# Kernel optimization log

Measured on AMD Instinct MI355X. Metric: run time of the kernel, lower is better.

The kernel has to match this reference:

```python
import jax, jax.numpy as jnp
import numpy as np

CW = 64            # channel_width; N = CW**2 = 4096 tokens = d_batch
BIAS = 1.0         # same_channel_bias
D_KQ = 2048
D_V = 2048
STEP = 0           # self.step at first call
T_IDX = 0          # self.t at first call
PE_N = 10000.0


def pe_row(t, d, n=PE_N):
    """Row t of the sinusoidal positional encoding P[t, :] of width d (d even)."""
    i = jnp.arange(d // 2, dtype=jnp.float32)
    denom = jnp.power(jnp.float32(n), 2.0 * i / d)
    ang = jnp.float32(t) / denom
    row = jnp.zeros((d,), dtype=jnp.float32)
    row = row.at[0::2].set(jnp.sin(ang)).at[1::2].set(jnp.cos(ang))
    return row


def setup_inputs() -> dict:
    key = jax.random.key(0)
    ks = jax.random.split(key, 6)
    N = CW * CW          # 4096
    d_in = 2048
    num_steps = 8
    return {
        "x": jax.random.normal(ks[0], (N, d_in), dtype=jnp.float32),
        "W_query": jax.random.uniform(ks[1], (d_in, D_KQ), dtype=jnp.float32),
        "W_key": jax.random.uniform(ks[2], (d_in, D_KQ), dtype=jnp.float32),
        "W_value": jax.random.uniform(ks[3], (d_in, D_V), dtype=jnp.float32),
        "b_channel": jax.random.uniform(ks[4], (N, D_V), dtype=jnp.float32),
        "b_t": jax.random.uniform(ks[5], (num_steps, N, D_V), dtype=jnp.float32),
    }


def reference(x, W_query, W_key, W_value, b_channel, b_t):
    N = x.shape[0]
    q = x @ W_query                      # [N, d_kq]
    k = x @ W_key                        # [N, d_kq]
    v = x @ W_value                      # [N, d_v]
    scores = q @ k.T                     # [N, N]
    # kron(eye(cw), ones(cw,cw)*bias): +bias where tokens share a channel block
    ch = jnp.arange(N) // CW
    scores = scores + jnp.where(ch[:, None] == ch[None, :], jnp.float32(BIAS), jnp.float32(0.0))
    # NOTE: bias added BEFORE the 1/sqrt(d_kq) scaling, as in the original
    attn = jax.nn.softmax(scores / jnp.float32(D_KQ) ** 0.5, axis=-1)
    ctx = attn @ v                       # [N, d_v]
    ctx = ctx + b_channel + b_t[STEP] + pe_row(T_IDX, D_V)
    return ctx
```

## Files before the change

### kernel.cpp

```cpp
#include <hip/hip_runtime.h>
#include <cstdint>
#include <cstddef>


using h8    = __attribute__((ext_vector_type(8))) _Float16;
using h4    = __attribute__((ext_vector_type(4))) _Float16;
using f32x4 = __attribute__((ext_vector_type(4))) float;

__device__ __forceinline__ void gll16(const void* g, void* l) {
  __builtin_amdgcn_global_load_lds(
      (const __attribute__((address_space(1))) uint32_t*)g,
      (__attribute__((address_space(3))) uint32_t*)l, 16, 0, 0);
}

__global__ __launch_bounds__(256) void split_x_kernel(
    const float* __restrict__ X, _Float16* __restrict__ hi,
    _Float16* __restrict__ lo, int n4)
{
  int i = blockIdx.x * 256 + threadIdx.x;
  if (i >= n4) return;
  float4 v = ((const float4*)X)[i];
  float a[4] = {v.x, v.y, v.z, v.w};
  h4 hh, ll;
#pragma unroll
  for (int e = 0; e < 4; ++e) {
    _Float16 h = (_Float16)a[e];
    hh[e] = h;
    ll[e] = (_Float16)(a[e] - (float)h);
  }
  ((h4*)hi)[i] = hh;
  ((h4*)lo)[i] = ll;
}

__global__ __launch_bounds__(256) void transpose_split_w(
    const float* __restrict__ W, _Float16* __restrict__ Thi,
    _Float16* __restrict__ Tlo, int D, int writeLo)
{
  __shared__ float t[32][33];
  int n0 = blockIdx.x * 32;
  int k0 = blockIdx.y * 32;
  int tx = threadIdx.x & 31;
  int ty = threadIdx.x >> 5;
  for (int j = ty; j < 32; j += 8)
    t[j][tx] = W[(size_t)(k0 + j) * D + n0 + tx];
  __syncthreads();
  for (int j = ty; j < 32; j += 8) {
    float v = t[tx][j];
    size_t o = (size_t)(n0 + j) * D + k0 + tx;
    _Float16 h = (_Float16)v;
    Thi[o] = h;
    if (writeLo) Tlo[o] = (_Float16)(v - (float)h);
  }
}

constexpr int EPI_QK = 0;
constexpr int EPI_VT = 1;
constexpr int EPI_S  = 2;
constexpr int EPI_CTX = 3;

template<int EPI, bool SPLIT>
__global__ __launch_bounds__(256, 2) void gemm_bt(
    const _Float16* __restrict__ A, const _Float16* __restrict__ Al,
    const _Float16* __restrict__ B, const _Float16* __restrict__ Bl,
    int K, int lda, int ldb, int ldc, int ldt,
    float* __restrict__ of32, _Float16* __restrict__ oh1,
    _Float16* __restrict__ oh2,
    const float* __restrict__ c1, const float* __restrict__ c2)
{
  __shared__ __align__(16) _Float16 sA [128 * 32];
  __shared__ __align__(16) _Float16 sB [128 * 32];
  __shared__ __align__(16) _Float16 sAl[SPLIT ? 128 * 32 : 8];
  __shared__ __align__(16) _Float16 sBl[SPLIT ? 128 * 32 : 8];

  const int tid  = threadIdx.x;
  const int lane = tid & 63;
  const int wave = tid >> 6;
  const int wm = wave >> 1, wn = wave & 1;
  const int m0 = blockIdx.y * 128, n0 = blockIdx.x * 128;

  const int ca = lane + 64 * wave;
  const int ra = ca >> 2, ka = (ca & 3) * 8;
  const int cc = ca + 256;
  const int rb = cc >> 2, kb = (cc & 3) * 8;
  const size_t lo0 = (size_t)wave * 1024;
  const size_t lo1 = lo0 + 4096;

  const _Float16* gA0 = A + (size_t)(m0 + ra) * lda + ka;
  const _Float16* gA1 = A + (size_t)(m0 + rb) * lda + kb;
  const _Float16* gB0 = B + (size_t)(n0 + ra) * ldb + ka;
  const _Float16* gB1 = B + (size_t)(n0 + rb) * ldb + kb;
  const _Float16* gAl0 = Al ? Al + (size_t)(m0 + ra) * lda + ka : nullptr;
  const _Float16* gAl1 = Al ? Al + (size_t)(m0 + rb) * lda + kb : nullptr;
  const _Float16* gBl0 = Bl ? Bl + (size_t)(n0 + ra) * ldb + ka : nullptr;
  const _Float16* gBl1 = Bl ? Bl + (size_t)(n0 + rb) * ldb + kb : nullptr;

  f32x4 acc[4][4];
#pragma unroll
  for (int i = 0; i < 4; ++i)
#pragma unroll
    for (int j = 0; j < 4; ++j) acc[i][j] = (f32x4){0.f, 0.f, 0.f, 0.f};

  const int fr = lane & 15;
  const int fk = (lane >> 4) * 8;

  for (int k0 = 0; k0 < K; k0 += 32) {
    gll16(gA0 + k0, (char*)sA + lo0);
    gll16(gA1 + k0, (char*)sA + lo1);
    gll16(gB0 + k0, (char*)sB + lo0);
    gll16(gB1 + k0, (char*)sB + lo1);
    if constexpr (SPLIT) {
      gll16(gAl0 + k0, (char*)sAl + lo0);
      gll16(gAl1 + k0, (char*)sAl + lo1);
      gll16(gBl0 + k0, (char*)sBl + lo0);
      gll16(gBl1 + k0, (char*)sBl + lo1);
    }
    __syncthreads();

    h8 af[4], bf[4], afl[4], bfl[4];
#pragma unroll
    for (int mi = 0; mi < 4; ++mi)
      af[mi] = *(const h8*)&sA[(wm * 64 + mi * 16 + fr) * 32 + fk];
#pragma unroll
    for (int ni = 0; ni < 4; ++ni)
      bf[ni] = *(const h8*)&sB[(wn * 64 + ni * 16 + fr) * 32 + fk];
    if constexpr (SPLIT) {
#pragma unroll
      for (int mi = 0; mi < 4; ++mi)
        afl[mi] = *(const h8*)&sAl[(wm * 64 + mi * 16 + fr) * 32 + fk];
#pragma unroll
      for (int ni = 0; ni < 4; ++ni)
        bfl[ni] = *(const h8*)&sBl[(wn * 64 + ni * 16 + fr) * 32 + fk];
    }

#pragma unroll
    for (int mi = 0; mi < 4; ++mi)
#pragma unroll
      for (int ni = 0; ni < 4; ++ni) {
        acc[mi][ni] = __builtin_amdgcn_mfma_f32_16x16x32_f16(
            af[mi], bf[ni], acc[mi][ni], 0, 0, 0);
        if constexpr (SPLIT) {
          acc[mi][ni] = __builtin_amdgcn_mfma_f32_16x16x32_f16(
              af[mi], bfl[ni], acc[mi][ni], 0, 0, 0);
          acc[mi][ni] = __builtin_amdgcn_mfma_f32_16x16x32_f16(
              afl[mi], bf[ni], acc[mi][ni], 0, 0, 0);
        }
      }
    __syncthreads();
  }

  const int drow = (lane >> 4) * 4;
  const int dcol = lane & 15;
#pragma unroll
  for (int mi = 0; mi < 4; ++mi) {
#pragma unroll
    for (int ni = 0; ni < 4; ++ni) {
      const int row = m0 + wm * 64 + mi * 16 + drow;
      const int col = n0 + wn * 64 + ni * 16 + dcol;
      f32x4 v = acc[mi][ni];
      if constexpr (EPI == EPI_S) {
#pragma unroll
        for (int r = 0; r < 4; ++r)
          of32[(size_t)(row + r) * ldc + col] = v[r];
      } else if constexpr (EPI == EPI_QK) {
#pragma unroll
        for (int r = 0; r < 4; ++r) {
          float x = v[r];
          _Float16 hh = (_Float16)x;
          size_t o = (size_t)(row + r) * ldc + col;
          oh1[o] = hh;
          oh2[o] = (_Float16)(x - (float)hh);
        }
      } else if constexpr (EPI == EPI_VT) {
        h4 hh;
#pragma unroll
        for (int r = 0; r < 4; ++r) hh[r] = (_Float16)v[r];
        *(h4*)&oh1[(size_t)col * ldt + row] = hh;
      } else {
#pragma unroll
        for (int r = 0; r < 4; ++r) {
          size_t o = (size_t)(row + r) * ldc + col;
          of32[o] = v[r] + c1[o] + c2[o] + ((col & 1) ? 1.0f : 0.0f);
        }
      }
    }
  }
}

template<int EPI, int NPASS>
__global__ __launch_bounds__(512, 2) void gemm256(
    const _Float16* __restrict__ A0, const _Float16* __restrict__ B0,
    const _Float16* __restrict__ A1, const _Float16* __restrict__ B1,
    const _Float16* __restrict__ A2, const _Float16* __restrict__ B2,
    int lda, int ldb, int ldc,
    float* __restrict__ of32, _Float16* __restrict__ oh1,
    _Float16* __restrict__ oh2)
{
  __shared__ __align__(16) char lds[147456];
  constexpr int T = NPASS * 32;

  const int tid  = threadIdx.x;
  const int lane = tid & 63;
  const int w    = tid >> 6;
  const int wm = w >> 2, wn = w & 3;
  const int fr = lane & 15, sl = lane >> 4;
  const int m0 = blockIdx.y * 256, n0 = blockIdx.x * 256;

  const int sswz  = ((sl ^ ((fr >> 1) & 3)) << 4);
  const int aBase = (wm * 128 + fr) * 64 + sswz;
  const int bBase = 65536 + (wn * 64 + fr) * 64 + sswz;
  const int rowoff = w * 16 + (lane >> 2);
  const int sL8 = ((lane & 3) ^ ((lane >> 3) & 3)) * 8;

  auto gstage = [&](int t, int isB, int kk) {
    const _Float16* g; int ld, r0, gk; char* dst;
    if (t >= T) {
      g = A0; ld = lda; r0 = m0; gk = 0; dst = lds + 131072;
    } else {
      const int p = t >> 5, kt = t & 31;
      g  = isB ? (p == 0 ? B0 : (p == 1 ? B1 : B2))
               : (p == 0 ? A0 : (p == 1 ? A1 : A2));
      ld = isB ? ldb : lda;
      r0 = isB ? n0 : m0;
      gk = kt * 64 + kk * 32;
      dst = lds + (isB ? 65536 : 0) + (t & 1) * 32768 + kk * 16384;
    }
#pragma unroll
    for (int i = 0; i < 2; ++i)
      gll16(g + (size_t)(r0 + i * 128 + rowoff) * ld + gk + sL8,
            dst + i * 8192 + w * 1024);
  };

  f32x4 acc[8][4];
#pragma unroll
  for (int i = 0; i < 8; ++i)
#pragma unroll
    for (int j = 0; j < 4; ++j) acc[i][j] = (f32x4){0.f, 0.f, 0.f, 0.f};

  gstage(0, 0, 0); gstage(0, 1, 0);
  gstage(0, 0, 1); gstage(0, 1, 1);
  gstage(1, 0, 0); gstage(1, 1, 0);
  asm volatile("s_waitcnt vmcnt(8)" ::: "memory");
  __builtin_amdgcn_sched_barrier(0);
  __builtin_amdgcn_s_barrier();

  h8 af[4], bf[4];
#pragma unroll 2
  for (int t = 0; t < T; ++t) {
    const char* aB = lds + (t & 1) * 32768;

#pragma unroll
    for (int i = 0; i < 4; ++i) af[i] = *(const h8*)(aB + aBase + i * 1024);
#pragma unroll
    for (int i = 0; i < 4; ++i) bf[i] = *(const h8*)(aB + bBase + i * 1024);
    gstage(t + 1, 0, 1);
    __builtin_amdgcn_s_barrier();
    asm volatile("s_waitcnt lgkmcnt(0)" ::: "memory");
    __builtin_amdgcn_sched_barrier(0);
    __builtin_amdgcn_s_setprio(1);
#pragma unroll
    for (int mi = 0; mi < 4; ++mi)
#pragma unroll
      for (int ni = 0; ni < 4; ++ni)
        acc[mi][ni] = __builtin_amdgcn_mfma_f32_16x16x32_f16(
            af[mi], bf[ni], acc[mi][ni], 0, 0, 0);
    __builtin_amdgcn_s_setprio(0);
    __builtin_amdgcn_s_barrier();

#pragma unroll
    for (int i = 0; i < 4; ++i)
      af[i] = *(const h8*)(aB + aBase + (4 + i) * 1024);
    gstage(t + 1, 1, 1);
    __builtin_amdgcn_s_barrier();
    asm volatile("s_waitcnt lgkmcnt(0)" ::: "memory");
    __builtin_amdgcn_sched_barrier(0);
    __builtin_amdgcn_s_setprio(1);
#pragma unroll
    for (int mi = 0; mi < 4; ++mi)
#pragma unroll
      for (int ni = 0; ni < 4; ++ni)
        acc[4 + mi][ni] = __builtin_amdgcn_mfma_f32_16x16x32_f16(
            af[mi], bf[ni], acc[4 + mi][ni], 0, 0, 0);
    __builtin_amdgcn_s_setprio(0);
    asm volatile("s_waitcnt vmcnt(8)" ::: "memory");
    __builtin_amdgcn_sched_barrier(0);
    __builtin_amdgcn_s_barrier();

#pragma unroll
    for (int i = 0; i < 4; ++i)
      af[i] = *(const h8*)(aB + 16384 + aBase + i * 1024);
#pragma unroll
    for (int i = 0; i < 4; ++i)
      bf[i] = *(const h8*)(aB + 16384 + bBase + i * 1024);
    gstage(t + 2, 0, 0);
    __builtin_amdgcn_s_barrier();
    asm volatile("s_waitcnt lgkmcnt(0)" ::: "memory");
    __builtin_amdgcn_sched_barrier(0);
    __builtin_amdgcn_s_setprio(1);
#pragma unroll
    for (int mi = 0; mi < 4; ++mi)
#pragma unroll
      for (int ni = 0; ni < 4; ++ni)
        acc[mi][ni] = __builtin_amdgcn_mfma_f32_16x16x32_f16(
            af[mi], bf[ni], acc[mi][ni], 0, 0, 0);
    __builtin_amdgcn_s_setprio(0);
    __builtin_amdgcn_s_barrier();

#pragma unroll
    for (int i = 0; i < 4; ++i)
      af[i] = *(const h8*)(aB + 16384 + aBase + (4 + i) * 1024);
    gstage(t + 2, 1, 0);
    __builtin_amdgcn_s_barrier();
    asm volatile("s_waitcnt lgkmcnt(0)" ::: "memory");
    __builtin_amdgcn_sched_barrier(0);
    __builtin_amdgcn_s_setprio(1);
#pragma unroll
    for (int mi = 0; mi < 4; ++mi)
#pragma unroll
      for (int ni = 0; ni < 4; ++ni)
        acc[4 + mi][ni] = __builtin_amdgcn_mfma_f32_16x16x32_f16(
            af[mi], bf[ni], acc[4 + mi][ni], 0, 0, 0);
    __builtin_amdgcn_s_setprio(0);
    asm volatile("s_waitcnt vmcnt(8)" ::: "memory");
    __builtin_amdgcn_sched_barrier(0);
    __builtin_amdgcn_s_barrier();
  }
  asm volatile("s_waitcnt vmcnt(0)" ::: "memory");

  const int drow = sl * 4;
#pragma unroll
  for (int mi = 0; mi < 8; ++mi) {
#pragma unroll
    for (int ni = 0; ni < 4; ++ni) {
      const int row = m0 + wm * 128 + mi * 16 + drow;
      const int col = n0 + wn * 64 + ni * 16 + fr;
      f32x4 v = acc[mi][ni];
      if constexpr (EPI == EPI_S) {
#pragma unroll
        for (int r = 0; r < 4; ++r)
          of32[(size_t)(row + r) * ldc + col] = v[r];
      } else {
#pragma unroll
        for (int r = 0; r < 4; ++r) {
          float x = v[r];
          _Float16 hh = (_Float16)x;
          size_t o = (size_t)(row + r) * ldc + col;
          oh1[o] = hh;
          oh2[o] = (_Float16)(x - (float)hh);
        }
      }
    }
  }
}

__global__ __launch_bounds__(256) void softmax_bias_kernel(
    float* __restrict__ S, int N)
{
  const float scale = 0.022097086912079608f;
  const int row = blockIdx.x;
  float* rp = S + (size_t)row * N;
  const int cblk = row & ~63;
  const int tid = threadIdx.x;

  float vals[16];
  float mx = -3.0e38f;
#pragma unroll
  for (int it = 0; it < 4; ++it) {
    int base = (it * 256 + tid) * 4;
    float4 v = *(const float4*)(rp + base);
    float a[4] = {v.x, v.y, v.z, v.w};
#pragma unroll
    for (int e = 0; e < 4; ++e) {
      int col = base + e;
      float s = a[e];
      if ((col & ~63) == cblk) s += 1.0f;
      s *= scale;
      vals[it * 4 + e] = s;
      mx = fmaxf(mx, s);
    }
  }
  __shared__ float red[8];
#pragma unroll
  for (int m = 32; m; m >>= 1) mx = fmaxf(mx, __shfl_xor(mx, m, 64));
  if ((tid & 63) == 0) red[tid >> 6] = mx;
  __syncthreads();
  mx = fmaxf(fmaxf(red[0], red[1]), fmaxf(red[2], red[3]));

  float sum = 0.f;
#pragma unroll
  for (int i = 0; i < 16; ++i) {
    float e = __expf(vals[i] - mx);
    vals[i] = e;
    sum += e;
  }
#pragma unroll
  for (int m = 32; m; m >>= 1) sum += __shfl_xor(sum, m, 64);
  if ((tid & 63) == 0) red[4 + (tid >> 6)] = sum;
  __syncthreads();
  sum = red[4] + red[5] + red[6] + red[7];
  float inv = 1.0f / sum;

  _Float16* op = (_Float16*)rp;
#pragma unroll
  for (int it = 0; it < 4; ++it) {
    int base = (it * 256 + tid) * 4;
    h4 hh;
#pragma unroll
    for (int e = 0; e < 4; ++e) hh[e] = (_Float16)(vals[it * 4 + e] * inv);
    *(h4*)(op + base) = hh;
  }
}

extern "C" void kernel_launch(void* const* d_in, const int* in_sizes, int n_in,
                              void* d_out, int out_size, void* d_ws,
                              size_t ws_size, hipStream_t stream)
{
  (void)in_sizes; (void)n_in; (void)out_size; (void)ws_size;
  const float* x   = (const float*)d_in[0];
  const float* Wq  = (const float*)d_in[1];
  const float* Wk  = (const float*)d_in[2];
  const float* Wv  = (const float*)d_in[3];
  const float* bch = (const float*)d_in[4];
  const float* bt0 = (const float*)d_in[5];
  float* out = (float*)d_out;

  char* ws = (char*)d_ws;
  const size_t O_XHI  = 0;
  const size_t O_XLO  = O_XHI + 16777216;
  const size_t O_WQKH = O_XLO + 16777216;
  const size_t O_WQKL = O_WQKH + 16777216;
  const size_t O_S    = 0;
  const size_t O_WVH  = 67108864;
  const size_t O_VT   = O_WVH + 8388608;
  const size_t O_QKH  = O_VT + 16777216;
  const size_t O_QKL  = O_QKH + 33554432;

  _Float16* xhi  = (_Float16*)(ws + O_XHI);
  _Float16* xlo  = (_Float16*)(ws + O_XLO);
  _Float16* wqkh = (_Float16*)(ws + O_WQKH);
  _Float16* wqkl = (_Float16*)(ws + O_WQKL);
  _Float16* wvh  = (_Float16*)(ws + O_WVH);
  _Float16* vT   = (_Float16*)(ws + O_VT);
  _Float16* qkh  = (_Float16*)(ws + O_QKH);
  _Float16* qkl  = (_Float16*)(ws + O_QKL);
  float*    S    = (float*)(ws + O_S);

  split_x_kernel<<<2097152 / 256, 256, 0, stream>>>(x, xhi, xlo, 2097152);
  dim3 tg(64, 64);
  transpose_split_w<<<tg, 256, 0, stream>>>(Wq, wqkh, wqkl, 2048, 1);
  transpose_split_w<<<tg, 256, 0, stream>>>(
      Wk, wqkh + (size_t)2048 * 2048, wqkl + (size_t)2048 * 2048, 2048, 1);
  transpose_split_w<<<tg, 256, 0, stream>>>(Wv, wvh, nullptr, 2048, 0);

  gemm256<EPI_QK, 3><<<dim3(16, 16), 512, 0, stream>>>(
      xhi, wqkh, xhi, wqkl, xlo, wqkh, 2048, 2048, 4096,
      nullptr, qkh, qkl);
  gemm_bt<EPI_VT, false><<<dim3(16, 32), 256, 0, stream>>>(
      xhi, nullptr, wvh, nullptr, 2048, 2048, 2048, 0, 4096,
      nullptr, vT, nullptr, nullptr, nullptr);

  gemm256<EPI_S, 3><<<dim3(16, 16), 512, 0, stream>>>(
      qkh, qkh + 2048, qkh, qkl + 2048, qkl, qkh + 2048, 4096, 4096, 4096,
      S, nullptr, nullptr);

  softmax_bias_kernel<<<4096, 256, 0, stream>>>(S, 4096);

  gemm_bt<EPI_CTX, false><<<dim3(16, 32), 256, 0, stream>>>(
      (const _Float16*)S, nullptr, vT, nullptr, 4096, 8192, 4096, 2048, 0,
      out, nullptr, nullptr, bch, bt0);
}
```

Before: 1.081 ms.

## Simplify GEMM main loop to two phases with fewer barriers

Replaces the hand-scheduled four-phase main loop with a two-phase loop per K-slab. Each phase issues both global-to-LDS stages up front, reads all 8 A and 4 B fragments, then runs 32 MFMAs. The sched_barriers, explicit lgkmcnt waits and half of the s_barriers are dropped, which cuts synchronisation and lets the compiler interleave LDS reads with MFMAs. In exchange it holds more fragment registers and gives up the explicit overlap control of the old schedule.

```diff
diff --git a/kernel.cpp b/kernel.cpp
--- a/kernel.cpp
+++ b/kernel.cpp
@@ -240,89 +240,38 @@
   gstage(0, 0, 1); gstage(0, 1, 1);
   gstage(1, 0, 0); gstage(1, 1, 0);
   asm volatile("s_waitcnt vmcnt(8)" ::: "memory");
-  __builtin_amdgcn_sched_barrier(0);
   __builtin_amdgcn_s_barrier();
 
-  h8 af[4], bf[4];
 #pragma unroll 2
   for (int t = 0; t < T; ++t) {
     const char* aB = lds + (t & 1) * 32768;
 
 #pragma unroll
-    for (int i = 0; i < 4; ++i) af[i] = *(const h8*)(aB + aBase + i * 1024);
-#pragma unroll
-    for (int i = 0; i < 4; ++i) bf[i] = *(const h8*)(aB + bBase + i * 1024);
-    gstage(t + 1, 0, 1);
-    __builtin_amdgcn_s_barrier();
-    asm volatile("s_waitcnt lgkmcnt(0)" ::: "memory");
-    __builtin_amdgcn_sched_barrier(0);
-    __builtin_amdgcn_s_setprio(1);
-#pragma unroll
-    for (int mi = 0; mi < 4; ++mi)
-#pragma unroll
-      for (int ni = 0; ni < 4; ++ni)
-        acc[mi][ni] = __builtin_amdgcn_mfma_f32_16x16x32_f16(
-            af[mi], bf[ni], acc[mi][ni], 0, 0, 0);
-    __builtin_amdgcn_s_setprio(0);
-    __builtin_amdgcn_s_barrier();
-
-#pragma unroll
-    for (int i = 0; i < 4; ++i)
-      af[i] = *(const h8*)(aB + aBase + (4 + i) * 1024);
-    gstage(t + 1, 1, 1);
-    __builtin_amdgcn_s_barrier();
-    asm volatile("s_waitcnt lgkmcnt(0)" ::: "memory");
-    __builtin_amdgcn_sched_barrier(0);
-    __builtin_amdgcn_s_setprio(1);
-#pragma unroll
-    for (int mi = 0; mi < 4; ++mi)
-#pragma unroll
-      for (int ni = 0; ni < 4; ++ni)
-        acc[4 + mi][ni] = __builtin_amdgcn_mfma_f32_16x16x32_f16(
-            af[mi], bf[ni], acc[4 + mi][ni], 0, 0, 0);
-    __builtin_amdgcn_s_setprio(0);
-    asm volatile("s_waitcnt vmcnt(8)" ::: "memory");
-    __builtin_amdgcn_sched_barrier(0);
-    __builtin_amdgcn_s_barrier();
-
-#pragma unroll
-    for (int i = 0; i < 4; ++i)
-      af[i] = *(const h8*)(aB + 16384 + aBase + i * 1024);
-#pragma unroll
-    for (int i = 0; i < 4; ++i)
-      bf[i] = *(const h8*)(aB + 16384 + bBase + i * 1024);
-    gstage(t + 2, 0, 0);
-    __builtin_amdgcn_s_barrier();
-    asm volatile("s_waitcnt lgkmcnt(0)" ::: "memory");
-    __builtin_amdgcn_sched_barrier(0);
-    __builtin_amdgcn_s_setprio(1);
-#pragma unroll
-    for (int mi = 0; mi < 4; ++mi)
-#pragma unroll
-      for (int ni = 0; ni < 4; ++ni)
-        acc[mi][ni] = __builtin_amdgcn_mfma_f32_16x16x32_f16(
-            af[mi], bf[ni], acc[mi][ni], 0, 0, 0);
-    __builtin_amdgcn_s_setprio(0);
-    __builtin_amdgcn_s_barrier();
-
-#pragma unroll
-    for (int i = 0; i < 4; ++i)
-      af[i] = *(const h8*)(aB + 16384 + aBase + (4 + i) * 1024);
-    gstage(t + 2, 1, 0);
-    __builtin_amdgcn_s_barrier();
-    asm volatile("s_waitcnt lgkmcnt(0)" ::: "memory");
-    __builtin_amdgcn_sched_barrier(0);
-    __builtin_amdgcn_s_setprio(1);
-#pragma unroll
-    for (int mi = 0; mi < 4; ++mi)
-#pragma unroll
-      for (int ni = 0; ni < 4; ++ni)
-        acc[4 + mi][ni] = __builtin_amdgcn_mfma_f32_16x16x32_f16(
-            af[mi], bf[ni], acc[4 + mi][ni], 0, 0, 0);
-    __builtin_amdgcn_s_setprio(0);
-    asm volatile("s_waitcnt vmcnt(8)" ::: "memory");
-    __builtin_amdgcn_sched_barrier(0);
-    __builtin_amdgcn_s_barrier();
+    for (int kk = 0; kk < 2; ++kk) {
+      if (kk == 0) { gstage(t + 1, 0, 1); gstage(t + 1, 1, 1); }
+      else         { gstage(t + 2, 0, 0); gstage(t + 2, 1, 0); }
+
+      const char* base = aB + kk * 16384;
+      h8 af[8], bf[4];
+#pragma unroll
+      for (int i = 0; i < 8; ++i)
+        af[i] = *(const h8*)(base + aBase + i * 1024);
+#pragma unroll
+      for (int i = 0; i < 4; ++i)
+        bf[i] = *(const h8*)(base + bBase + i * 1024);
+
+      __builtin_amdgcn_s_setprio(1);
+#pragma unroll
+      for (int mi = 0; mi < 8; ++mi)
+#pragma unroll
+        for (int ni = 0; ni < 4; ++ni)
+          acc[mi][ni] = __builtin_amdgcn_mfma_f32_16x16x32_f16(
+              af[mi], bf[ni], acc[mi][ni], 0, 0, 0);
+      __builtin_amdgcn_s_setprio(0);
+
+      asm volatile("s_waitcnt vmcnt(8)" ::: "memory");
+      __builtin_amdgcn_s_barrier();
+    }
   }
   asm volatile("s_waitcnt vmcnt(0)" ::: "memory");
 
```

Result: faster. 932.5 us (-13.7%).
